# Optimization experiments

Hardware: AMD Instinct MI355X
Metric: run time of the kernel (lower is better)

## Reference

```python
import jax, jax.numpy as jnp
import numpy as np

N = 50000      # nodes in current tree level
N_CH = 3       # actual children present in mailbox
D = 4          # max_output_degree
H = 256        # h_size


def setup_inputs() -> dict:
    key = jax.random.key(0)
    ks = jax.random.split(key, 6)
    return {
        "neighbour_h": jax.random.normal(ks[0], (N, N_CH, H), dtype=jnp.float32),
        "neighbour_c": jax.random.normal(ks[1], (N, N_CH, H), dtype=jnp.float32),
        "f_input": jax.random.normal(ks[2], (N, H), dtype=jnp.float32),
        "iou_input": jax.random.normal(ks[3], (N, 3 * H), dtype=jnp.float32),
        # torch nn.Linear convention: weight [out, in]; one per child position
        "U_f": jax.random.normal(ks[4], (D, H, H), dtype=jnp.float32) * 0.05,
        "U_iou": jax.random.normal(ks[5], (D, 3 * H, H), dtype=jnp.float32) * 0.05,
    }


def reference(neighbour_h, neighbour_c, f_input, iou_input, U_f, U_iou):
    n, n_ch, h = neighbour_h.shape
    d = U_f.shape[0]
    pad = d - n_ch
    # check_missing_children: pad with bottom_h / bottom_c == zeros
    nh = jnp.pad(neighbour_h, ((0, 0), (0, pad), (0, 0)))  # [N, D, H]
    nc = jnp.pad(neighbour_c, ((0, 0), (0, pad), (0, 0)))  # [N, D, H]
    # per-position forget gates: U_f_i @ h_i, plus f_input repeated per child
    f_logits = jnp.einsum('ndh,dkh->ndk', nh, U_f) + f_input[:, None, :]
    # iou gate (canonical n-ary tree-LSTM): sum_i U_iou_i @ h_i, plus iou_input
    iou_aggr = jnp.einsum('ndh,dkh->nk', nh, U_iou) + iou_input  # [N, 3H]
    f = jax.nn.sigmoid(f_logits)
    c_aggr = jnp.sum(f * nc, axis=1)  # [N, H]
    # apply_node_func: iou = iou_input + iou_aggr (iou_input counted twice, as in source)
    iou = iou_input + iou_aggr
    i, o, u = jnp.split(iou, 3, axis=1)
    c = jax.nn.sigmoid(i) * jnp.tanh(u) + c_aggr
    h_out = jax.nn.sigmoid(o) * jnp.tanh(c)
    return (h_out, c)
```

## Files before the change

### kernel.cpp

```cpp
#include <hip/hip_runtime.h>
#include <cstdint>
#include <cstddef>

#define NN 50000
#define HD 256
#define NCH 3

typedef __attribute__((ext_vector_type(8))) short shortx8;
typedef __attribute__((ext_vector_type(4))) float floatx4;
typedef __attribute__((ext_vector_type(16))) float floatx16;

__device__ __forceinline__ unsigned short f2bf(float x) {
    union { float f; uint32_t u; } v; v.f = x;
    uint32_t r = v.u + 0x7fffu + ((v.u >> 16) & 1u);
    return (unsigned short)(r >> 16);
}
__device__ __forceinline__ float bf2f(unsigned short u) {
    union { uint32_t u; float f; } v; v.u = ((uint32_t)u) << 16; return v.f;
}
__device__ __forceinline__ uint32_t cvtpk(float a, float b) {
    uint32_t r;
    asm("v_cvt_pk_bf16_f32 %0, %1, %2" : "=v"(r) : "v"(a), "v"(b));
    return r;
}
__device__ __forceinline__ float sigf(float x) {
    return 1.0f / (1.0f + __expf(-x));
}
__device__ __forceinline__ float tanhfast(float x) {
    return 1.0f - 2.0f / (__expf(2.0f * x) + 1.0f);
}
__device__ __forceinline__ floatx16 mfma32(shortx8 a, shortx8 b, floatx16 c) {
    return __builtin_amdgcn_mfma_f32_32x32x16_bf16(a, b, c, 0, 0, 0);
}
__device__ __forceinline__ void glds16(const void* g, void* l) {
    __builtin_amdgcn_global_load_lds(
        (const __attribute__((address_space(1))) void*)g,
        (__attribute__((address_space(3))) void*)l, 16, 0, 0);
}

__global__ void prep_split(const float* __restrict__ U_f,
                           const float* __restrict__ U_iou,
                           unsigned short* __restrict__ wsB) {
    int idx  = blockIdx.x * 256 + threadIdx.x;
    int lane = idx & 63;
    int fg   = idx >> 6;
    const float* src;
    if (fg < 384) {
        int t   = fg >> 4;
        int ksl = fg & 15;
        int d   = t >> 3;
        int c   = t * 32 + (lane & 31) - d * 256;
        int kk  = ksl * 16 + (lane >> 5) * 8;
        src = U_f + ((size_t)d * 256 + c) * 256 + kk;
    } else {
        int fg2 = fg - 384;
        int t2  = fg2 / 48;
        int ksl = fg2 % 48;
        int gc  = t2 * 32 + (lane & 31);
        int g   = gc >> 8;
        int c   = gc & 255;
        int k   = ksl * 16 + (lane >> 5) * 8;
        int d   = k >> 8;
        int kk  = k & 255;
        src = U_iou + ((size_t)d * 768 + g * 256 + c) * 256 + kk;
    }
    shortx8 o;
    #pragma unroll
    for (int e = 0; e < 8; ++e) o[e] = (short)f2bf(src[e]);
    reinterpret_cast<shortx8*>(wsB)[idx] = o;
}

__global__ __launch_bounds__(256) void conv_nh(
    const float* __restrict__ nh, unsigned short* __restrict__ dst,
    int base, int count)
{
    int total = count * 96;
    for (int id = blockIdx.x * 256 + threadIdx.x; id < total;
         id += gridDim.x * 256) {
        int r = id / 96;
        int q = id - r * 96;
        const float4* s4 = reinterpret_cast<const float4*>(
            nh + (size_t)(base + r) * 768 + q * 8);
        float4 a = s4[0], b = s4[1];
        union { uint32_t u[4]; shortx8 v; } o;
        o.u[0] = cvtpk(a.x, a.y); o.u[1] = cvtpk(a.z, a.w);
        o.u[2] = cvtpk(b.x, b.y); o.u[3] = cvtpk(b.z, b.w);
        int S = q >> 3, c = q & 7;
        *reinterpret_cast<shortx8*>(
            dst + (size_t)r * 768 + S * 64 + ((c ^ (r & 7)) * 8)) = o.v;
    }
}

__global__ __launch_bounds__(512, 4) void gemm_logits(
    const unsigned short* __restrict__ nhb,
    const unsigned short* __restrict__ wsB,
    unsigned short* __restrict__ logits,
    int count)
{
    __shared__ unsigned short nhT[128 * 64];
    __shared__ unsigned short wT[32 * 512];

    const int tid = threadIdx.x;
    const int bid = blockIdx.x;
    const int cb  = bid % 6;
    const int mb  = bid / 6;
    const int nbl = mb * 128;

    const int lane = tid & 63;
    const int cg   = tid >> 6;
    const int nl   = lane & 31;
    const int hi   = lane >> 5;

    const bool isF    = (cb < 3);
    const int  kbase  = isF ? cb * 256 : 0;
    const int  nsteps = isF ? 4 : 12;
    const int  tF  = cb * 8 + cg;
    const int  t2  = (cb - 3) * 8 + cg;
    const int  fragbase = isF ? (tF * 16) : (384 + t2 * 48);
    const int  colbase  = (isF ? (tF * 32) : (768 + t2 * 32)) + hi * 4;
    const int  clim = count - 1;

    floatx16 acc[4];
    #pragma unroll
    for (int nt = 0; nt < 4; ++nt)
        #pragma unroll
        for (int t = 0; t < 16; ++t) acc[nt][t] = 0.0f;

    for (int s = 0; s < nsteps; ++s) {
        #pragma unroll
        for (int jj = 0; jj < 2; ++jj) {
            int j    = cg * 2 + jj;
            int el   = j * 64 + lane;
            int node = el >> 3;
            int kk8  = (el & 7) * 8;
            int row  = nbl + node; if (row > clim) row = clim;
            glds16(nhb + (size_t)row * 768 + kbase + s * 64 + kk8,
                   (void*)(nhT + j * 512));
        }
        #pragma unroll
        for (int jj = 0; jj < 4; ++jj) {
            int frag = fragbase + s * 4 + jj;
            glds16(wsB + (size_t)frag * 512 + lane * 8,
                   (void*)(wT + (cg * 4 + jj) * 512));
        }
        __syncthreads();

        #pragma unroll
        for (int it = 0; it < 4; ++it) {
            shortx8 a = *reinterpret_cast<const shortx8*>(
                wT + (cg * 4 + it) * 512 + lane * 8);
            int ch = it * 2 + hi;
            #pragma unroll
            for (int nt = 0; nt < 4; ++nt) {
                int nd = nt * 32 + nl;
                shortx8 b = *reinterpret_cast<const shortx8*>(
                    nhT + nd * 64 + ((ch ^ (nl & 7)) * 8));
                acc[nt] = mfma32(a, b, acc[nt]);
            }
        }
        __syncthreads();
    }

    #pragma unroll
    for (int nt = 0; nt < 4; ++nt) {
        int row = nbl + nt * 32 + nl;
        if (row < count) {
            unsigned short* lr = logits + (size_t)row * 1536;
            #pragma unroll
            for (int q = 0; q < 4; ++q) {
                uint2 wv;
                wv.x = cvtpk(acc[nt][q * 4 + 0], acc[nt][q * 4 + 1]);
                wv.y = cvtpk(acc[nt][q * 4 + 2], acc[nt][q * 4 + 3]);
                *reinterpret_cast<uint2*>(lr + colbase + q * 8) = wv;
            }
        }
    }
}

__global__ __launch_bounds__(256) void ew_kernel(
    const unsigned short* __restrict__ logits,
    const float* __restrict__ ncc,
    const float* __restrict__ f_in,
    const float* __restrict__ iou_in,
    float* __restrict__ out,
    int node_base, int count)
{
    int total = count * 64;
    for (int id = blockIdx.x * 256 + threadIdx.x; id < total;
         id += gridDim.x * 256) {
        int row = id >> 6;
        int col = (id & 63) * 4;
        int gn  = node_base + row;
        const unsigned short* lr = logits + (size_t)row * 1536;

        floatx4 fi = *reinterpret_cast<const floatx4*>(
            f_in + (size_t)gn * HD + col);
        float cagg[4] = {0.f, 0.f, 0.f, 0.f};
        #pragma unroll
        for (int d = 0; d < 3; ++d) {
            ushort4 fb = *reinterpret_cast<const ushort4*>(lr + d * 256 + col);
            floatx4 nc4 = *reinterpret_cast<const floatx4*>(
                ncc + (size_t)gn * 768 + d * 256 + col);
            cagg[0] += sigf(bf2f(fb.x) + fi[0]) * nc4[0];
            cagg[1] += sigf(bf2f(fb.y) + fi[1]) * nc4[1];
            cagg[2] += sigf(bf2f(fb.z) + fi[2]) * nc4[2];
            cagg[3] += sigf(bf2f(fb.w) + fi[3]) * nc4[3];
        }
        ushort4 ib = *reinterpret_cast<const ushort4*>(lr +  768 + col);
        ushort4 ob = *reinterpret_cast<const ushort4*>(lr + 1024 + col);
        ushort4 ub = *reinterpret_cast<const ushort4*>(lr + 1280 + col);
        size_t iob = (size_t)gn * 768 + col;
        floatx4 i4 = *reinterpret_cast<const floatx4*>(iou_in + iob);
        floatx4 o4 = *reinterpret_cast<const floatx4*>(iou_in + iob + 256);
        floatx4 u4 = *reinterpret_cast<const floatx4*>(iou_in + iob + 512);
        float iv[4] = {bf2f(ib.x), bf2f(ib.y), bf2f(ib.z), bf2f(ib.w)};
        float ov[4] = {bf2f(ob.x), bf2f(ob.y), bf2f(ob.z), bf2f(ob.w)};
        float uv[4] = {bf2f(ub.x), bf2f(ub.y), bf2f(ub.z), bf2f(ub.w)};
        floatx4 cc, hh;
        #pragma unroll
        for (int r = 0; r < 4; ++r) {
            float c = sigf(iv[r] + 2.0f * i4[r]) * tanhfast(uv[r] + 2.0f * u4[r])
                      + cagg[r];
            cc[r] = c;
            hh[r] = sigf(ov[r] + 2.0f * o4[r]) * tanhfast(c);
        }
        *reinterpret_cast<floatx4*>(out + (size_t)gn * HD + col) = hh;
        *reinterpret_cast<floatx4*>(out + (size_t)(NN + gn) * HD + col) = cc;
    }
}

__global__ void prep_fused32(const float* __restrict__ U_f,
                             const float* __restrict__ U_iou,
                             unsigned short* __restrict__ wsB) {
    int idx = blockIdx.x * 256 + threadIdx.x;
    int lane = idx & 63;
    int ks   = (idx >> 6) & 15;
    int tile = (idx >> 10) & 31;
    int d    = idx >> 15;
    if (d >= NCH) return;
    int col = tile * 32 + (lane & 31);
    int k0  = ks * 16 + (lane >> 5) * 8;
    const float* src = (col < 256)
        ? (U_f   + (((size_t)d * 256 + col)         * 256 + k0))
        : (U_iou + (((size_t)d * 768 + (col - 256)) * 256 + k0));
    shortx8 o;
    #pragma unroll
    for (int e = 0; e < 8; ++e) o[e] = (short)f2bf(src[e]);
    reinterpret_cast<shortx8*>(wsB)[idx] = o;
}

__global__ __launch_bounds__(512, 4) void fused_main(
    const float* __restrict__ nh, const float* __restrict__ ncc,
    const float* __restrict__ f_in, const float* __restrict__ iou_in,
    const unsigned short* __restrict__ wsB, float* __restrict__ out)
{
    __shared__ unsigned short sA[NCH * 32 * 32 * 8];
    const int tid  = threadIdx.x;
    const int nb   = blockIdx.x * 32;
    const int lane = tid & 63;
    const int cg   = tid >> 6;
    const int nl   = lane & 31;
    const int hi   = lane >> 5;
    const int colb = cg * 32 + hi * 4;
    const shortx8* Bfr = reinterpret_cast<const shortx8*>(wsB);
    #pragma unroll
    for (int i = 0; i < 6; ++i) {
        int c = i * 512 + tid;
        int d = c >> 10, node = (c >> 5) & 31, slot = c & 31;
        int gn = nb + node;
        shortx8 o;
        if (gn < NN) {
            const float4* q = reinterpret_cast<const float4*>(
                nh + ((size_t)gn * (NCH * HD) + d * HD + slot * 8));
            float4 a = q[0], b = q[1];
            union { uint32_t u[4]; shortx8 v; } t;
            t.u[0] = cvtpk(a.x, a.y); t.u[1] = cvtpk(a.z, a.w);
            t.u[2] = cvtpk(b.x, b.y); t.u[3] = cvtpk(b.z, b.w);
            o = t.v;
        } else {
            for (int e = 0; e < 8; ++e) o[e] = 0;
        }
        int idx = (d * 32 + node) * 32 + (slot ^ (node & 7));
        *reinterpret_cast<shortx8*>(&sA[idx * 8]) = o;
    }
    __syncthreads();
    const int  n     = nb + nl;
    const bool valid = (n < NN);
    const int  nc_   = valid ? n : (NN - 1);
    ushort4 finb[4];
    #pragma unroll
    for (int q = 0; q < 4; ++q) {
        floatx4 v = *reinterpret_cast<const floatx4*>(
            f_in + (size_t)nc_ * HD + colb + q * 8);
        finb[q] = ushort4{f2bf(v[0]), f2bf(v[1]), f2bf(v[2]), f2bf(v[3])};
    }
    float cagg[16];
    #pragma unroll
    for (int t = 0; t < 16; ++t) cagg[t] = 0.0f;
    floatx16 accI, accO, accU;
    #pragma unroll
    for (int t = 0; t < 16; ++t) { accI[t] = 0.f; accO[t] = 0.f; accU[t] = 0.f; }
    const int nsw = nl & 7;
    #pragma unroll 1
    for (int d = 0; d < NCH; ++d) {
        floatx16 accF;
        #pragma unroll
        for (int t = 0; t < 16; ++t) accF[t] = 0.0f;
        #pragma unroll 2
        for (int ks = 0; ks < 16; ++ks) {
            shortx8 aF = Bfr[((d * 32 +      cg) * 16 + ks) * 64 + lane];
            shortx8 aI = Bfr[((d * 32 +  8 + cg) * 16 + ks) * 64 + lane];
            shortx8 aO = Bfr[((d * 32 + 16 + cg) * 16 + ks) * 64 + lane];
            shortx8 aU = Bfr[((d * 32 + 24 + cg) * 16 + ks) * 64 + lane];
            int ch = (ks * 2 + hi) ^ nsw;
            shortx8 b = *reinterpret_cast<const shortx8*>(
                &sA[((d * 32 + nl) * 32 + ch) * 8]);
            accF = mfma32(aF, b, accF);
            accI = mfma32(aI, b, accI);
            accO = mfma32(aO, b, accO);
            accU = mfma32(aU, b, accU);
        }
        #pragma unroll
        for (int q = 0; q < 4; ++q) {
            floatx4 ncr = *reinterpret_cast<const floatx4*>(
                ncc + (size_t)nc_ * (NCH * HD) + d * HD + colb + q * 8);
            cagg[q*4+0] += sigf(accF[q*4+0] + bf2f(finb[q].x)) * ncr[0];
            cagg[q*4+1] += sigf(accF[q*4+1] + bf2f(finb[q].y)) * ncr[1];
            cagg[q*4+2] += sigf(accF[q*4+2] + bf2f(finb[q].z)) * ncr[2];
            cagg[q*4+3] += sigf(accF[q*4+3] + bf2f(finb[q].w)) * ncr[3];
        }
    }
    if (valid) {
        #pragma unroll
        for (int q = 0; q < 4; ++q) {
            int col = colb + q * 8;
            size_t base = (size_t)n * 768 + col;
            floatx4 i4 = *reinterpret_cast<const floatx4*>(iou_in + base);
            floatx4 o4 = *reinterpret_cast<const floatx4*>(iou_in + base + 256);
            floatx4 u4 = *reinterpret_cast<const floatx4*>(iou_in + base + 512);
            floatx4 cc, hh;
            #pragma unroll
            for (int r = 0; r < 4; ++r) {
                int t = q * 4 + r;
                float c = sigf(accI[t] + 2.f*i4[r]) * tanhfast(accU[t] + 2.f*u4[r])
                          + cagg[t];
                cc[r] = c;
                hh[r] = sigf(accO[t] + 2.f*o4[r]) * tanhfast(c);
            }
            *reinterpret_cast<floatx4*>(out + (size_t)n * HD + col) = hh;
            *reinterpret_cast<floatx4*>(out + (size_t)(NN + n) * HD + col) = cc;
        }
    }
}

extern "C" void kernel_launch(void* const* d_in, const int* in_sizes, int n_in,
                              void* d_out, int out_size, void* d_ws, size_t ws_size,
                              hipStream_t stream) {
    const float* nh     = (const float*)d_in[0];
    const float* ncc    = (const float*)d_in[1];
    const float* f_in   = (const float*)d_in[2];
    const float* iou_in = (const float*)d_in[3];
    const float* U_f    = (const float*)d_in[4];
    const float* U_iou  = (const float*)d_in[5];
    unsigned short* wsB = (unsigned short*)d_ws;

    const size_t FRAG_BYTES = (size_t)98304 * 16;
    const size_t DATA_OFF   = (size_t)2 << 20;

    long long cmax = 0;
    if (ws_size > DATA_OFF)
        cmax = (long long)((ws_size - DATA_OFF) / 4608);
    cmax = (cmax / 128) * 128;

    if (cmax >= 128) {
        hipLaunchKernelGGL(prep_split, dim3(384), dim3(256), 0, stream,
                           U_f, U_iou, wsB);
        unsigned short* nhswz  = (unsigned short*)((char*)d_ws + DATA_OFF);
        unsigned short* logits = nhswz + (size_t)cmax * 768;
        int base = 0;
        while (base < NN) {
            long long rem = NN - base;
            int count = (int)(rem < cmax ? rem : cmax);

            int cgrid = (count * 96 + 255) / 256;
            if (cgrid > 2048) cgrid = 2048;
            hipLaunchKernelGGL(conv_nh, dim3(cgrid), dim3(256), 0, stream,
                               nh, nhswz, base, count);

            int nmb = (count + 127) / 128;
            hipLaunchKernelGGL(gemm_logits, dim3(nmb * 6), dim3(512), 0,
                               stream, nhswz, wsB, logits, count);

            int ewgrid = (count * 64 + 255) / 256;
            if (ewgrid > 2048) ewgrid = 2048;
            hipLaunchKernelGGL(ew_kernel, dim3(ewgrid), dim3(256), 0, stream,
                               logits, ncc, f_in, iou_in, (float*)d_out,
                               base, count);
            base += count;
        }
    } else if (ws_size >= FRAG_BYTES) {
        hipLaunchKernelGGL(prep_fused32, dim3(384), dim3(256), 0, stream,
                           U_f, U_iou, wsB);
        hipLaunchKernelGGL(fused_main, dim3((NN + 31) / 32), dim3(512), 0,
                           stream, nh, ncc, f_in, iou_in, wsB, (float*)d_out);
    }
}
```

Baseline: 303.9 us.

## Double-buffer node tiles in LDS and prefetch weight fragments into registers

```diff
diff --git a/kernel.cpp b/kernel.cpp
--- a/kernel.cpp
+++ b/kernel.cpp
@@ -97,8 +97,7 @@
     unsigned short* __restrict__ logits,
     int count)
 {
-    __shared__ unsigned short nhT[128 * 64];
-    __shared__ unsigned short wT[32 * 512];
+    __shared__ unsigned short nhT[2][128 * 64];
 
     const int tid = threadIdx.x;
     const int bid = blockIdx.x;
@@ -126,40 +125,55 @@
         #pragma unroll
         for (int t = 0; t < 16; ++t) acc[nt][t] = 0.0f;
 
+#define STAGE_NH(S, B)                                                       \
+    {                                                                        \
+        _Pragma("unroll")                                                    \
+        for (int jj = 0; jj < 2; ++jj) {                                     \
+            int j    = cg * 2 + jj;                                          \
+            int el   = j * 64 + lane;                                        \
+            int node = el >> 3;                                               \
+            int kk8  = (el & 7) * 8;                                          \
+            int row  = nbl + node; if (row > clim) row = clim;               \
+            glds16(nhb + (size_t)row * 768 + kbase + (S) * 64 + kk8,         \
+                   (void*)(nhT[(B)] + j * 512));                             \
+        }                                                                    \
+    }
+
+    shortx8 wcur[4], wnxt[4];
+    STAGE_NH(0, 0);
+    #pragma unroll
+    for (int jj = 0; jj < 4; ++jj)
+        wcur[jj] = *reinterpret_cast<const shortx8*>(
+            wsB + (size_t)(fragbase + jj) * 512 + lane * 8);
+    __syncthreads();
+
     for (int s = 0; s < nsteps; ++s) {
-        #pragma unroll
-        for (int jj = 0; jj < 2; ++jj) {
-            int j    = cg * 2 + jj;
-            int el   = j * 64 + lane;
-            int node = el >> 3;
-            int kk8  = (el & 7) * 8;
-            int row  = nbl + node; if (row > clim) row = clim;
-            glds16(nhb + (size_t)row * 768 + kbase + s * 64 + kk8,
-                   (void*)(nhT + j * 512));
-        }
-        #pragma unroll
-        for (int jj = 0; jj < 4; ++jj) {
-            int frag = fragbase + s * 4 + jj;
-            glds16(wsB + (size_t)frag * 512 + lane * 8,
-                   (void*)(wT + (cg * 4 + jj) * 512));
-        }
-        __syncthreads();
-
+        if (s + 1 < nsteps) {
+            STAGE_NH(s + 1, (s + 1) & 1);
+            #pragma unroll
+            for (int jj = 0; jj < 4; ++jj)
+                wnxt[jj] = *reinterpret_cast<const shortx8*>(
+                    wsB + (size_t)(fragbase + (s + 1) * 4 + jj) * 512 + lane * 8);
+        }
+
+        const unsigned short* buf = nhT[s & 1];
         #pragma unroll
         for (int it = 0; it < 4; ++it) {
-            shortx8 a = *reinterpret_cast<const shortx8*>(
-                wT + (cg * 4 + it) * 512 + lane * 8);
+            shortx8 a = wcur[it];
             int ch = it * 2 + hi;
             #pragma unroll
             for (int nt = 0; nt < 4; ++nt) {
                 int nd = nt * 32 + nl;
                 shortx8 b = *reinterpret_cast<const shortx8*>(
-                    nhT + nd * 64 + ((ch ^ (nl & 7)) * 8));
+                    buf + nd * 64 + ((ch ^ (nl & 7)) * 8));
                 acc[nt] = mfma32(a, b, acc[nt]);
             }
         }
         __syncthreads();
-    }
+        #pragma unroll
+        for (int jj = 0; jj < 4; ++jj) wcur[jj] = wnxt[jj];
+    }
+#undef STAGE_NH
 
     #pragma unroll
     for (int nt = 0; nt < 4; ++nt) {
```

After: 302.1 us. Within noise of the previous version (-0.6%).

## Fuse GEMM and elementwise epilogue into one kernel, dropping bf16 logits buffer

Applied to the files above, without the earlier changes.

```diff
diff --git a/kernel.cpp b/kernel.cpp
--- a/kernel.cpp
+++ b/kernel.cpp
@@ -38,32 +38,20 @@
         (__attribute__((address_space(3))) void*)l, 16, 0, 0);
 }
 
-__global__ void prep_split(const float* __restrict__ U_f,
-                           const float* __restrict__ U_iou,
-                           unsigned short* __restrict__ wsB) {
-    int idx  = blockIdx.x * 256 + threadIdx.x;
+__global__ void prep_fused32(const float* __restrict__ U_f,
+                             const float* __restrict__ U_iou,
+                             unsigned short* __restrict__ wsB) {
+    int idx = blockIdx.x * 256 + threadIdx.x;
     int lane = idx & 63;
-    int fg   = idx >> 6;
-    const float* src;
-    if (fg < 384) {
-        int t   = fg >> 4;
-        int ksl = fg & 15;
-        int d   = t >> 3;
-        int c   = t * 32 + (lane & 31) - d * 256;
-        int kk  = ksl * 16 + (lane >> 5) * 8;
-        src = U_f + ((size_t)d * 256 + c) * 256 + kk;
-    } else {
-        int fg2 = fg - 384;
-        int t2  = fg2 / 48;
-        int ksl = fg2 % 48;
-        int gc  = t2 * 32 + (lane & 31);
-        int g   = gc >> 8;
-        int c   = gc & 255;
-        int k   = ksl * 16 + (lane >> 5) * 8;
-        int d   = k >> 8;
-        int kk  = k & 255;
-        src = U_iou + ((size_t)d * 768 + g * 256 + c) * 256 + kk;
-    }
+    int ks   = (idx >> 6) & 15;
+    int tile = (idx >> 10) & 31;
+    int d    = idx >> 15;
+    if (d >= NCH) return;
+    int col = tile * 32 + (lane & 31);
+    int k0  = ks * 16 + (lane >> 5) * 8;
+    const float* src = (col < 256)
+        ? (U_f   + (((size_t)d * 256 + col)         * 256 + k0))
+        : (U_iou + (((size_t)d * 768 + (col - 256)) * 256 + k0));
     shortx8 o;
     #pragma unroll
     for (int e = 0; e < 8; ++e) o[e] = (short)f2bf(src[e]);
@@ -91,162 +79,107 @@
     }
 }
 
-__global__ __launch_bounds__(512, 4) void gemm_logits(
+__global__ __launch_bounds__(512, 4) void fused_v2(
     const unsigned short* __restrict__ nhb,
+    const float* __restrict__ ncc,
+    const float* __restrict__ f_in,
+    const float* __restrict__ iou_in,
     const unsigned short* __restrict__ wsB,
-    unsigned short* __restrict__ logits,
-    int count)
+    float* __restrict__ out,
+    int base, int count)
 {
-    __shared__ unsigned short nhT[128 * 64];
-    __shared__ unsigned short wT[32 * 512];
-
-    const int tid = threadIdx.x;
-    const int bid = blockIdx.x;
-    const int cb  = bid % 6;
-    const int mb  = bid / 6;
-    const int nbl = mb * 128;
-
+    __shared__ unsigned short sA[NCH * 32 * 32 * 8];
+    const int tid  = threadIdx.x;
+    const int lb   = blockIdx.x * 32;
     const int lane = tid & 63;
     const int cg   = tid >> 6;
     const int nl   = lane & 31;
     const int hi   = lane >> 5;
-
-    const bool isF    = (cb < 3);
-    const int  kbase  = isF ? cb * 256 : 0;
-    const int  nsteps = isF ? 4 : 12;
-    const int  tF  = cb * 8 + cg;
-    const int  t2  = (cb - 3) * 8 + cg;
-    const int  fragbase = isF ? (tF * 16) : (384 + t2 * 48);
-    const int  colbase  = (isF ? (tF * 32) : (768 + t2 * 32)) + hi * 4;
-    const int  clim = count - 1;
-
-    floatx16 acc[4];
-    #pragma unroll
-    for (int nt = 0; nt < 4; ++nt)
-        #pragma unroll
-        for (int t = 0; t < 16; ++t) acc[nt][t] = 0.0f;
-
-    for (int s = 0; s < nsteps; ++s) {
-        #pragma unroll
-        for (int jj = 0; jj < 2; ++jj) {
-            int j    = cg * 2 + jj;
-            int el   = j * 64 + lane;
-            int node = el >> 3;
-            int kk8  = (el & 7) * 8;
-            int row  = nbl + node; if (row > clim) row = clim;
-            glds16(nhb + (size_t)row * 768 + kbase + s * 64 + kk8,
-                   (void*)(nhT + j * 512));
-        }
-        #pragma unroll
-        for (int jj = 0; jj < 4; ++jj) {
-            int frag = fragbase + s * 4 + jj;
-            glds16(wsB + (size_t)frag * 512 + lane * 8,
-                   (void*)(wT + (cg * 4 + jj) * 512));
-        }
-        __syncthreads();
-
-        #pragma unroll
-        for (int it = 0; it < 4; ++it) {
-            shortx8 a = *reinterpret_cast<const shortx8*>(
-                wT + (cg * 4 + it) * 512 + lane * 8);
-            int ch = it * 2 + hi;
+    const int colb = cg * 32 + hi * 4;
+    const shortx8* Bfr = reinterpret_cast<const shortx8*>(wsB);
+
+    #pragma unroll
+    for (int j = 0; j < 6; ++j) {
+        int ri = j * 8 + cg;
+        int d  = ri >> 4;
+        int np = ri & 15;
+        int r  = lb + 2 * np + (lane >> 5);
+        if (r > count - 1) r = count - 1;
+        glds16(nhb + (size_t)r * 768 + d * 256 + (lane & 31) * 8,
+               (void*)(sA + ri * 512));
+    }
+    __syncthreads();
+
+    const int  ln    = lb + nl;
+    const bool valid = (ln < count);
+    const int  n     = base + ln;
+    const int  nc_   = valid ? n : base;
+
+    ushort4 finb[4];
+    #pragma unroll
+    for (int q = 0; q < 4; ++q) {
+        floatx4 v = *reinterpret_cast<const floatx4*>(
+            f_in + (size_t)nc_ * HD + colb + q * 8);
+        finb[q] = ushort4{f2bf(v[0]), f2bf(v[1]), f2bf(v[2]), f2bf(v[3])};
+    }
+    float cagg[16];
+    #pragma unroll
+    for (int t = 0; t < 16; ++t) cagg[t] = 0.0f;
+    floatx16 accI, accO, accU;
+    #pragma unroll
+    for (int t = 0; t < 16; ++t) { accI[t] = 0.f; accO[t] = 0.f; accU[t] = 0.f; }
+    const int nsw = nl & 7;
+
+    #pragma unroll 1
+    for (int d = 0; d < NCH; ++d) {
+        floatx16 accF;
+        #pragma unroll
+        for (int t = 0; t < 16; ++t) accF[t] = 0.0f;
+        #pragma unroll 2
+        for (int ks = 0; ks < 16; ++ks) {
+            shortx8 aF = Bfr[((d * 32 +      cg) * 16 + ks) * 64 + lane];
+            shortx8 aI = Bfr[((d * 32 +  8 + cg) * 16 + ks) * 64 + lane];
+            shortx8 aO = Bfr[((d * 32 + 16 + cg) * 16 + ks) * 64 + lane];
+            shortx8 aU = Bfr[((d * 32 + 24 + cg) * 16 + ks) * 64 + lane];
+            int ch = (ks * 2 + hi) ^ nsw;
+            shortx8 b = *reinterpret_cast<const shortx8*>(
+                &sA[((d * 32 + nl) * 32 + ch) * 8]);
+            accF = mfma32(aF, b, accF);
+            accI = mfma32(aI, b, accI);
+            accO = mfma32(aO, b, accO);
+            accU = mfma32(aU, b, accU);
+        }
+        #pragma unroll
+        for (int q = 0; q < 4; ++q) {
+            floatx4 ncr = *reinterpret_cast<const floatx4*>(
+                ncc + (size_t)nc_ * (NCH * HD) + d * HD + colb + q * 8);
+            cagg[q*4+0] += sigf(accF[q*4+0] + bf2f(finb[q].x)) * ncr[0];
+            cagg[q*4+1] += sigf(accF[q*4+1] + bf2f(finb[q].y)) * ncr[1];
+            cagg[q*4+2] += sigf(accF[q*4+2] + bf2f(finb[q].z)) * ncr[2];
+            cagg[q*4+3] += sigf(accF[q*4+3] + bf2f(finb[q].w)) * ncr[3];
+        }
+    }
+    if (valid) {
+        #pragma unroll
+        for (int q = 0; q < 4; ++q) {
+            int col = colb + q * 8;
+            size_t b2 = (size_t)n * 768 + col;
+            floatx4 i4 = *reinterpret_cast<const floatx4*>(iou_in + b2);
+            floatx4 o4 = *reinterpret_cast<const floatx4*>(iou_in + b2 + 256);
+            floatx4 u4 = *reinterpret_cast<const floatx4*>(iou_in + b2 + 512);
+            floatx4 cc, hh;
             #pragma unroll
-            for (int nt = 0; nt < 4; ++nt) {
-                int nd = nt * 32 + nl;
-                shortx8 b = *reinterpret_cast<const shortx8*>(
-                    nhT + nd * 64 + ((ch ^ (nl & 7)) * 8));
-                acc[nt] = mfma32(a, b, acc[nt]);
+            for (int r = 0; r < 4; ++r) {
+                int t = q * 4 + r;
+                float c = sigf(accI[t] + 2.f*i4[r]) * tanhfast(accU[t] + 2.f*u4[r])
+                          + cagg[t];
+                cc[r] = c;
+                hh[r] = sigf(accO[t] + 2.f*o4[r]) * tanhfast(c);
             }
-        }
-        __syncthreads();
-    }
-
-    #pragma unroll
-    for (int nt = 0; nt < 4; ++nt) {
-        int row = nbl + nt * 32 + nl;
-        if (row < count) {
-            unsigned short* lr = logits + (size_t)row * 1536;
-            #pragma unroll
-            for (int q = 0; q < 4; ++q) {
-                uint2 wv;
-                wv.x = cvtpk(acc[nt][q * 4 + 0], acc[nt][q * 4 + 1]);
-                wv.y = cvtpk(acc[nt][q * 4 + 2], acc[nt][q * 4 + 3]);
-                *reinterpret_cast<uint2*>(lr + colbase + q * 8) = wv;
-            }
-        }
-    }
-}
-
-__global__ __launch_bounds__(256) void ew_kernel(
-    const unsigned short* __restrict__ logits,
-    const float* __restrict__ ncc,
-    const float* __restrict__ f_in,
-    const float* __restrict__ iou_in,
-    float* __restrict__ out,
-    int node_base, int count)
-{
-    int total = count * 64;
-    for (int id = blockIdx.x * 256 + threadIdx.x; id < total;
-         id += gridDim.x * 256) {
-        int row = id >> 6;
-        int col = (id & 63) * 4;
-        int gn  = node_base + row;
-        const unsigned short* lr = logits + (size_t)row * 1536;
-
-        floatx4 fi = *reinterpret_cast<const floatx4*>(
-            f_in + (size_t)gn * HD + col);
-        float cagg[4] = {0.f, 0.f, 0.f, 0.f};
-        #pragma unroll
-        for (int d = 0; d < 3; ++d) {
-            ushort4 fb = *reinterpret_cast<const ushort4*>(lr + d * 256 + col);
-            floatx4 nc4 = *reinterpret_cast<const floatx4*>(
-                ncc + (size_t)gn * 768 + d * 256 + col);
-            cagg[0] += sigf(bf2f(fb.x) + fi[0]) * nc4[0];
-            cagg[1] += sigf(bf2f(fb.y) + fi[1]) * nc4[1];
-            cagg[2] += sigf(bf2f(fb.z) + fi[2]) * nc4[2];
-            cagg[3] += sigf(bf2f(fb.w) + fi[3]) * nc4[3];
-        }
-        ushort4 ib = *reinterpret_cast<const ushort4*>(lr +  768 + col);
-        ushort4 ob = *reinterpret_cast<const ushort4*>(lr + 1024 + col);
-        ushort4 ub = *reinterpret_cast<const ushort4*>(lr + 1280 + col);
-        size_t iob = (size_t)gn * 768 + col;
-        floatx4 i4 = *reinterpret_cast<const floatx4*>(iou_in + iob);
-        floatx4 o4 = *reinterpret_cast<const floatx4*>(iou_in + iob + 256);
-        floatx4 u4 = *reinterpret_cast<const floatx4*>(iou_in + iob + 512);
-        float iv[4] = {bf2f(ib.x), bf2f(ib.y), bf2f(ib.z), bf2f(ib.w)};
-        float ov[4] = {bf2f(ob.x), bf2f(ob.y), bf2f(ob.z), bf2f(ob.w)};
-        float uv[4] = {bf2f(ub.x), bf2f(ub.y), bf2f(ub.z), bf2f(ub.w)};
-        floatx4 cc, hh;
-        #pragma unroll
-        for (int r = 0; r < 4; ++r) {
-            float c = sigf(iv[r] + 2.0f * i4[r]) * tanhfast(uv[r] + 2.0f * u4[r])
-                      + cagg[r];
-            cc[r] = c;
-            hh[r] = sigf(ov[r] + 2.0f * o4[r]) * tanhfast(c);
-        }
-        *reinterpret_cast<floatx4*>(out + (size_t)gn * HD + col) = hh;
-        *reinterpret_cast<floatx4*>(out + (size_t)(NN + gn) * HD + col) = cc;
-    }
-}
-
-__global__ void prep_fused32(const float* __restrict__ U_f,
-                             const float* __restrict__ U_iou,
-                             unsigned short* __restrict__ wsB) {
-    int idx = blockIdx.x * 256 + threadIdx.x;
-    int lane = idx & 63;
-    int ks   = (idx >> 6) & 15;
-    int tile = (idx >> 10) & 31;
-    int d    = idx >> 15;
-    if (d >= NCH) return;
-    int col = tile * 32 + (lane & 31);
-    int k0  = ks * 16 + (lane >> 5) * 8;
-    const float* src = (col < 256)
-        ? (U_f   + (((size_t)d * 256 + col)         * 256 + k0))
-        : (U_iou + (((size_t)d * 768 + (col - 256)) * 256 + k0));
-    shortx8 o;
-    #pragma unroll
-    for (int e = 0; e < 8; ++e) o[e] = (short)f2bf(src[e]);
-    reinterpret_cast<shortx8*>(wsB)[idx] = o;
+            *reinterpret_cast<floatx4*>(out + (size_t)n * HD + col) = hh;
+            *reinterpret_cast<floatx4*>(out + (size_t)(NN + n) * HD + col) = cc;
+        }
+    }
 }
 
 __global__ __launch_bounds__(512, 4) void fused_main(
@@ -334,10 +267,10 @@
         #pragma unroll
         for (int q = 0; q < 4; ++q) {
             int col = colb + q * 8;
-            size_t base = (size_t)n * 768 + col;
-            floatx4 i4 = *reinterpret_cast<const floatx4*>(iou_in + base);
-            floatx4 o4 = *reinterpret_cast<const floatx4*>(iou_in + base + 256);
-            floatx4 u4 = *reinterpret_cast<const floatx4*>(iou_in + base + 512);
+            size_t b2 = (size_t)n * 768 + col;
+            floatx4 i4 = *reinterpret_cast<const floatx4*>(iou_in + b2);
+            floatx4 o4 = *reinterpret_cast<const floatx4*>(iou_in + b2 + 256);
+            floatx4 u4 = *reinterpret_cast<const floatx4*>(iou_in + b2 + 512);
             floatx4 cc, hh;
             #pragma unroll
             for (int r = 0; r < 4; ++r) {
@@ -369,14 +302,13 @@
 
     long long cmax = 0;
     if (ws_size > DATA_OFF)
-        cmax = (long long)((ws_size - DATA_OFF) / 4608);
+        cmax = (long long)((ws_size - DATA_OFF) / 1536);
     cmax = (cmax / 128) * 128;
 
     if (cmax >= 128) {
-        hipLaunchKernelGGL(prep_split, dim3(384), dim3(256), 0, stream,
+        hipLaunchKernelGGL(prep_fused32, dim3(384), dim3(256), 0, stream,
                            U_f, U_iou, wsB);
-        unsigned short* nhswz  = (unsigned short*)((char*)d_ws + DATA_OFF);
-        unsigned short* logits = nhswz + (size_t)cmax * 768;
+        unsigned short* nhb = (unsigned short*)((char*)d_ws + DATA_OFF);
         int base = 0;
         while (base < NN) {
             long long rem = NN - base;
@@ -385,17 +317,11 @@
             int cgrid = (count * 96 + 255) / 256;
             if (cgrid > 2048) cgrid = 2048;
             hipLaunchKernelGGL(conv_nh, dim3(cgrid), dim3(256), 0, stream,
-                               nh, nhswz, base, count);
-
-            int nmb = (count + 127) / 128;
-            hipLaunchKernelGGL(gemm_logits, dim3(nmb * 6), dim3(512), 0,
-                               stream, nhswz, wsB, logits, count);
-
-            int ewgrid = (count * 64 + 255) / 256;
-            if (ewgrid > 2048) ewgrid = 2048;
-            hipLaunchKernelGGL(ew_kernel, dim3(ewgrid), dim3(256), 0, stream,
-                               logits, ncc, f_in, iou_in, (float*)d_out,
-                               base, count);
+                               nh, nhb, base, count);
+
+            hipLaunchKernelGGL(fused_v2, dim3((count + 31) / 32), dim3(512), 0,
+                               stream, nhb, ncc, f_in, iou_in, wsB,
+                               (float*)d_out, base, count);
             base += count;
         }
     } else if (ws_size >= FRAG_BYTES) {
```

New measurement: 312.1 us. 2.7% more time.
